# Optimization experiments

Measured on AMD Instinct MI355X. Metric: run time of the kernel, lower is better.

## Reference

```python
import jax, jax.numpy as jnp
import numpy as np

WH, WW = 16, 16          # window size
S = WH * WW              # tokens per window = 256
B = 128                  # batch of windows
E = 1024                 # embed_dim
H = 16                   # num_heads
D = E // H               # head_dim = 64


def _swin_rel_index():
    # Swin-style relative position index, identical to the torch buffer construction
    coords = np.stack(np.meshgrid(np.arange(WH), np.arange(WW), indexing='ij'))  # [2,WH,WW]
    cf = coords.reshape(2, -1)                         # [2, S]
    rel = cf[:, :, None] - cf[:, None, :]              # [2, S, S]
    rel = rel.transpose(1, 2, 0).copy()                # [S, S, 2]
    rel[..., 0] += WH - 1
    rel[..., 1] += WW - 1
    rel[..., 0] *= 2 * WW - 1
    return rel.sum(-1).astype(np.int32)                # [S, S] in [0, (2WH-1)(2WW-1))


def setup_inputs() -> dict:
    key = jax.random.key(0)
    ks = jax.random.split(key, 6)
    x = jax.random.normal(ks[0], (B, S, E), dtype=jnp.float32)
    qkv_w = jax.random.normal(ks[1], (3 * E, E), dtype=jnp.float32) * 0.02
    qkv_b = jax.random.normal(ks[2], (3 * E,), dtype=jnp.float32) * 0.02
    out_w = jax.random.normal(ks[3], (E, E), dtype=jnp.float32) * 0.02
    out_b = jax.random.normal(ks[4], (E,), dtype=jnp.float32) * 0.02
    bias_table = jax.random.normal(ks[5], ((2 * WH - 1) * (2 * WW - 1), H), dtype=jnp.float32) * 0.02
    rel_index = jnp.asarray(_swin_rel_index())
    return {"x": x, "qkv_w": qkv_w, "qkv_b": qkv_b, "out_w": out_w,
            "out_b": out_b, "bias_table": bias_table, "rel_index": rel_index,
            "x_ignored_": 0, "x_ignored_1_": 0}


def reference(x, qkv_w, qkv_b, out_w, out_b, bias_table, rel_index, x_ignored_, x_ignored_1_):
    b, s, e = x.shape
    h = bias_table.shape[-1]
    d = e // h
    # fused QKV projection
    qkv = x @ qkv_w.T + qkv_b                          # [b, s, 3e]
    qkv = qkv.reshape(b, s, 3, h, d)
    q, k, v = qkv[:, :, 0], qkv[:, :, 1], qkv[:, :, 2]  # [b, s, h, d]
    scale = d ** -0.5
    # learned relative position bias, [h, s, s]
    bias = bias_table[rel_index.reshape(-1)].reshape(s, s, h).transpose(2, 0, 1)
    scores = jnp.einsum('bqhd,bkhd->bhqk', q, k) * scale + bias[None]
    attn = jax.nn.softmax(scores, axis=-1)
    ctx = jnp.einsum('bhqk,bkhd->bqhd', attn, v).reshape(b, s, e)
    return ctx @ out_w.T + out_b
```

## Files before the change

### kernel.cpp

```cpp
#include <hip/hip_runtime.h>
#include <stdint.h>

#define BB 128
#define SS 256
#define EE 1024
#define HH 16
#define DD 64
#define MM (BB*SS)

#define LOG2E 1.44269504088896f

typedef __attribute__((ext_vector_type(8))) short bf16x8;
typedef __attribute__((ext_vector_type(4))) float f32x4;

__device__ __forceinline__ unsigned short f2bf(float f) {
  union { float f; unsigned int u; } c; c.f = f;
  unsigned int u = c.u;
  u += 0x7fffu + ((u >> 16) & 1u);
  return (unsigned short)(u >> 16);
}

__device__ __forceinline__ float fast_exp2(float x) {
#if __has_builtin(__builtin_amdgcn_exp2f)
  return __builtin_amdgcn_exp2f(x);
#else
  return exp2f(x);
#endif
}

__device__ __forceinline__ float fast_rcp(float x) {
#if __has_builtin(__builtin_amdgcn_rcpf)
  return __builtin_amdgcn_rcpf(x);
#else
  return 1.0f / x;
#endif
}

__device__ __forceinline__ void gld16(const unsigned short* g, unsigned short* l) {
  __builtin_amdgcn_global_load_lds((__attribute__((address_space(1))) void*)(g),
                                   (__attribute__((address_space(3))) void*)(l), 16, 0, 0);
}

__global__ __launch_bounds__(256) void prep_kernel(const float4* __restrict__ x4,
                                                   const float4* __restrict__ qw,
                                                   const float4* __restrict__ ow,
                                                   const float* __restrict__ btab,
                                                   const int* __restrict__ ridx,
                                                   ushort4* __restrict__ xb,
                                                   ushort4* __restrict__ qwb,
                                                   ushort4* __restrict__ owb,
                                                   float* __restrict__ biasC) {
  const int NX = (MM * EE) / 4;
  const int NQ = (3 * EE * EE) / 4;
  const int NO = (EE * EE) / 4;
  const int NBIAS = HH * SS * SS;
  const int total = NX + NQ + NO + NBIAS;
  int stride = gridDim.x * blockDim.x;
  for (int i = blockIdx.x * blockDim.x + threadIdx.x; i < total; i += stride) {
    if (i < NX) {
      float4 v = x4[i];
      ushort4 r; r.x = f2bf(v.x); r.y = f2bf(v.y); r.z = f2bf(v.z); r.w = f2bf(v.w);
      xb[i] = r;
    } else if (i < NX + NQ) {
      int t = i - NX;
      float4 v = qw[t];
      ushort4 r; r.x = f2bf(v.x); r.y = f2bf(v.y); r.z = f2bf(v.z); r.w = f2bf(v.w);
      qwb[t] = r;
    } else if (i < NX + NQ + NO) {
      int t = i - (NX + NQ);
      float4 v = ow[t];
      ushort4 r; r.x = f2bf(v.x); r.y = f2bf(v.y); r.z = f2bf(v.z); r.w = f2bf(v.w);
      owb[t] = r;
    } else {
      int t = i - (NX + NQ + NO);
      int h   = t >> 16;
      int row = (t >> 8) & 255;
      int lo  = (t >> 4) & 15;
      int hi  = t & 15;
      int col = hi * 16 + lo;
      biasC[t] = btab[ridx[row * SS + col] * HH + h] * LOG2E;
    }
  }
}

#define GEMM_NT 16

__device__ __forceinline__ void mfma16(f32x4& c, bf16x8 a, bf16x8 b) {
  c = __builtin_amdgcn_mfma_f32_16x16x32_bf16(a, b, c, 0, 0, 0);
}

#define STAGE_A(buf, kh, tt) do { \
    unsigned short* _d = S_A + ((buf)*2 + (kh))*8192; \
    gld16(srcA0 + (tt)*64 + (kh)*32, _d + ldso0); \
    gld16(srcA1 + (tt)*64 + (kh)*32, _d + ldso1); } while (0)
#define STAGE_B(buf, kh, tt) do { \
    unsigned short* _d = S_B + ((buf)*2 + (kh))*8192; \
    gld16(srcB0 + (tt)*64 + (kh)*32, _d + ldso0); \
    gld16(srcB1 + (tt)*64 + (kh)*32, _d + ldso1); } while (0)
#define LOAD_A8(buf, kh) do { \
    const unsigned short* _u = S_A + ((buf)*2 + (kh))*8192 + aoff; \
    _Pragma("unroll") for (int mi = 0; mi < 8; ++mi) \
      af[mi] = *(const bf16x8*)(_u + mi*512); } while (0)
#define LOAD_B2(buf, kh, nj0) do { \
    const unsigned short* _u = S_B + ((buf)*2 + (kh))*8192 + boff; \
    bfr[(nj0)]   = *(const bf16x8*)(_u + (nj0)*512); \
    bfr[(nj0)+1] = *(const bf16x8*)(_u + ((nj0)+1)*512); } while (0)
#define MFMA_Q(nj0) do { \
    _Pragma("unroll") for (int mi = 0; mi < 8; ++mi) { \
      mfma16(acc[mi][(nj0)],   af[mi], bfr[(nj0)]); \
      mfma16(acc[mi][(nj0)+1], af[mi], bfr[(nj0)+1]); } } while (0)
#define WAIT_LGKM0() do { asm volatile("s_waitcnt lgkmcnt(0)" ::: "memory"); \
                          __builtin_amdgcn_sched_barrier(0); } while (0)

__device__ __forceinline__ void gemm256_loop(const unsigned short* __restrict__ A,
                                             const unsigned short* __restrict__ Bw,
                                             unsigned short* S_A, unsigned short* S_B,
                                             int row0, int col0, f32x4 (&acc)[8][4]) {
  const int tid = threadIdx.x;
  const int wave = tid >> 6, lane = tid & 63;
  const int wm = wave >> 2, wn = wave & 3;
  const int l15 = lane & 15, quad = lane >> 4;
  const int cq = quad ^ ((l15 >> 1) & 3);
  const int aoff = (wm * 128 + l15) * 32 + cq * 8;
  const int boff = (wn * 64 + l15) * 32 + cq * 8;
  const int r0g = tid >> 2, c0g = tid & 3;
  const int gc = c0g ^ ((r0g >> 1) & 3);
  const unsigned short* srcA0 = A  + (size_t)(row0 + r0g) * EE + gc * 8;
  const unsigned short* srcA1 = A  + (size_t)(row0 + 128 + r0g) * EE + gc * 8;
  const unsigned short* srcB0 = Bw + (size_t)(col0 + r0g) * EE + gc * 8;
  const unsigned short* srcB1 = Bw + (size_t)(col0 + 128 + r0g) * EE + gc * 8;
  const int ldso0 = wave * 512;
  const int ldso1 = 4096 + wave * 512;

  STAGE_A(0, 0, 0); STAGE_B(0, 0, 0); STAGE_A(0, 1, 0); STAGE_B(0, 1, 0);
  STAGE_A(1, 0, 1); STAGE_B(1, 0, 1); STAGE_A(1, 1, 1);
  asm volatile("s_waitcnt vmcnt(6)" ::: "memory");
  __builtin_amdgcn_sched_barrier(0);
  __builtin_amdgcn_s_barrier();

  bf16x8 af[8], bfr[4];
  for (int t = 0; t < GEMM_NT; ++t) {
    const int d = t & 1;
    LOAD_A8(d, 0); LOAD_B2(d, 0, 0);
    if (t + 1 < GEMM_NT) STAGE_B(d ^ 1, 1, t + 1);
    __builtin_amdgcn_s_barrier();
    WAIT_LGKM0();
    __builtin_amdgcn_s_setprio(1);
    MFMA_Q(0);
    __builtin_amdgcn_s_setprio(0);
    __builtin_amdgcn_s_barrier();
    LOAD_B2(d, 0, 2);
    if (t + 2 < GEMM_NT) STAGE_A(d, 0, t + 2);
    __builtin_amdgcn_s_barrier();
    WAIT_LGKM0();
    __builtin_amdgcn_s_setprio(1);
    MFMA_Q(2);
    __builtin_amdgcn_s_setprio(0);
    __builtin_amdgcn_s_barrier();
    LOAD_A8(d, 1); LOAD_B2(d, 1, 0);
    if (t + 2 < GEMM_NT) STAGE_B(d, 0, t + 2);
    __builtin_amdgcn_s_barrier();
    WAIT_LGKM0();
    __builtin_amdgcn_s_setprio(1);
    MFMA_Q(0);
    __builtin_amdgcn_s_setprio(0);
    __builtin_amdgcn_s_barrier();
    LOAD_B2(d, 1, 2);
    if (t + 2 < GEMM_NT) STAGE_A(d, 1, t + 2);
    if (t < GEMM_NT - 2) { asm volatile("s_waitcnt vmcnt(6)" ::: "memory"); }
    else                 { asm volatile("s_waitcnt vmcnt(0)" ::: "memory"); }
    __builtin_amdgcn_sched_barrier(0);
    __builtin_amdgcn_s_barrier();
    WAIT_LGKM0();
    __builtin_amdgcn_s_setprio(1);
    MFMA_Q(2);
    __builtin_amdgcn_s_setprio(0);
    __builtin_amdgcn_s_barrier();
  }
}

__global__ __launch_bounds__(512, 2) void qkv_gemm(const unsigned short* __restrict__ A,
                                                   const unsigned short* __restrict__ Bw,
                                                   const float* __restrict__ bias,
                                                   unsigned short* __restrict__ q,
                                                   unsigned short* __restrict__ kx,
                                                   unsigned short* __restrict__ vt) {
  __shared__ unsigned short S_A[32768];
  __shared__ unsigned short S_B[32768];
  const int bid = blockIdx.x;
  const int swz = (bid & 7) * (gridDim.x >> 3) + (bid >> 3);
  const int row0 = (swz & 127) * 256;
  const int col0 = (swz >> 7) * 256;
  const int tid = threadIdx.x;
  const int wave = tid >> 6, lane = tid & 63;
  const int wm = wave >> 2, wn = wave & 3;
  const int l15 = lane & 15, quad = lane >> 4;
  f32x4 acc[8][4];
#pragma unroll
  for (int i = 0; i < 8; ++i)
#pragma unroll
    for (int j = 0; j < 4; ++j) acc[i][j] = (f32x4){0.f, 0.f, 0.f, 0.f};
  gemm256_loop(A, Bw, S_A, S_B, row0, col0, acc);
  const int which = col0 >> 10;
  const float QS = 0.125f * LOG2E;
#pragma unroll
  for (int mi = 0; mi < 8; ++mi) {
    const int m = row0 + wm * 128 + mi * 16 + quad * 4;
    const int bb = m >> 8;
    const int s0 = m & 255;
#pragma unroll
    for (int nj = 0; nj < 4; ++nj) {
      const int n = col0 + wn * 64 + nj * 16 + l15;
      const int hn = (n >> 6) & 15;
      const int dd2 = n & 63;
      const float bv = bias[n];
      if (which == 0) {
        size_t base = ((size_t)(bb * HH + hn) * SS + s0) * DD + dd2;
#pragma unroll
        for (int r = 0; r < 4; ++r)
          q[base + (size_t)r * DD] = f2bf((acc[mi][nj][r] + bv) * QS);
      } else if (which == 1) {
        size_t base = ((size_t)(bb * HH + hn) * SS + s0) * DD + dd2;
#pragma unroll
        for (int r = 0; r < 4; ++r)
          kx[base + (size_t)r * DD] = f2bf(acc[mi][nj][r] + bv);
      } else {
        size_t base = ((size_t)(bb * HH + hn) * DD + dd2) * SS + s0;
        ushort4 pk;
        pk.x = f2bf(acc[mi][nj][0] + bv);
        pk.y = f2bf(acc[mi][nj][1] + bv);
        pk.z = f2bf(acc[mi][nj][2] + bv);
        pk.w = f2bf(acc[mi][nj][3] + bv);
        *(ushort4*)(vt + base) = pk;
      }
    }
  }
}

__global__ __launch_bounds__(256) void attn_kernel(const unsigned short* __restrict__ q,
                                                   const unsigned short* __restrict__ kx,
                                                   const unsigned short* __restrict__ vt,
                                                   const float* __restrict__ biasC,
                                                   unsigned short* __restrict__ ctx) {
  __shared__ unsigned short Ks[256 * 64];
  __shared__ unsigned short P[4][16 * 256];
  const int tid = threadIdx.x;
  const int wave = tid >> 6, lane = tid & 63;
  const int l15 = lane & 15, quad = lane >> 4;
  const int swl = l15 & 7;
  const int bh = blockIdx.x;
  const int h = bh & 15;
  const int b_ = bh >> 4;
  const unsigned short* qp = q + (size_t)bh * SS * DD;
  const unsigned short* kp = kx + (size_t)bh * SS * DD;
  const unsigned short* vp = vt + (size_t)bh * SS * DD;

#pragma unroll
  for (int rr = 0; rr < 8; ++rr) {
    int gc = rr * 256 + tid;
    int row = gc >> 3, sc = gc & 7;
    int c = sc ^ (row & 7);
    gld16(kp + row * 64 + c * 8, Ks + (rr * 256 + wave * 64) * 8);
  }
  __syncthreads();

  unsigned short* Pw = &P[wave][0];
  for (int qblk = 0; qblk < 4; ++qblk) {
    const int qr0 = qblk * 64 + wave * 16;
    bf16x8 aq0 = *(const bf16x8*)(qp + (qr0 + l15) * DD + quad * 8);
    bf16x8 aq1 = *(const bf16x8*)(qp + (qr0 + l15) * DD + 32 + quad * 8);

    f32x4 sacc[16];
#pragma unroll
    for (int j = 0; j < 16; ++j) sacc[j] = (f32x4){0.f, 0.f, 0.f, 0.f};
#pragma unroll
    for (int j = 0; j < 16; ++j) {
      const unsigned short* krow = Ks + (j * 16 + l15) * 64;
      bf16x8 b0 = *(const bf16x8*)(krow + (quad ^ swl) * 8);
      bf16x8 b1 = *(const bf16x8*)(krow + ((4 + quad) ^ swl) * 8);
      sacc[j] = __builtin_amdgcn_mfma_f32_16x16x32_bf16(aq0, b0, sacc[j], 0, 0, 0);
      sacc[j] = __builtin_amdgcn_mfma_f32_16x16x32_bf16(aq1, b1, sacc[j], 0, 0, 0);
    }
#pragma unroll
    for (int r = 0; r < 4; ++r) {
      const int prow = quad * 4 + r;
      const float* bC = biasC + ((size_t)((h * 256 + qr0 + prow) * 16 + l15)) * 16;
      float4 bv0 = ((const float4*)bC)[0];
      float4 bv1 = ((const float4*)bC)[1];
      float4 bv2 = ((const float4*)bC)[2];
      float4 bv3 = ((const float4*)bC)[3];
      float bj[16] = {bv0.x, bv0.y, bv0.z, bv0.w, bv1.x, bv1.y, bv1.z, bv1.w,
                      bv2.x, bv2.y, bv2.z, bv2.w, bv3.x, bv3.y, bv3.z, bv3.w};
      float s = 0.f;
#pragma unroll
      for (int j = 0; j < 16; ++j) {
        float e = fast_exp2(sacc[j][r] + bj[j]);
        sacc[j][r] = e;
        s += e;
      }
#pragma unroll
      for (int m = 8; m >= 1; m >>= 1) s += __shfl_xor(s, m, 16);
      float rs = fast_rcp(s);
      const int psw = prow & 7;
#pragma unroll
      for (int j = 0; j < 16; ++j) {
        union { float f; unsigned int u; } cv; cv.f = sacc[j][r] * rs;
        unsigned short pb = (unsigned short)((cv.u + 0x8000u) >> 16);
        Pw[prow * 256 + (((2 * j + (l15 >> 3)) ^ psw) << 3) + swl] = pb;
      }
    }
    f32x4 cacc[4];
#pragma unroll
    for (int nt = 0; nt < 4; ++nt) cacc[nt] = (f32x4){0.f, 0.f, 0.f, 0.f};
#pragma unroll
    for (int kk = 0; kk < 8; ++kk) {
      bf16x8 a = *(const bf16x8*)(Pw + l15 * 256 + (((kk * 4 + quad) ^ swl) << 3));
#pragma unroll
      for (int nt = 0; nt < 4; ++nt) {
        bf16x8 b = *(const bf16x8*)(vp + (nt * 16 + l15) * SS + kk * 32 + quad * 8);
        cacc[nt] = __builtin_amdgcn_mfma_f32_16x16x32_bf16(a, b, cacc[nt], 0, 0, 0);
      }
    }
#pragma unroll
    for (int nt = 0; nt < 4; ++nt)
#pragma unroll
      for (int r = 0; r < 4; ++r)
        ctx[(size_t)(b_ * SS + qr0 + quad * 4 + r) * EE + h * DD + nt * 16 + l15] =
            f2bf(cacc[nt][r]);
  }
}

__global__ __launch_bounds__(512, 2) void out_gemm(const unsigned short* __restrict__ A,
                                                   const unsigned short* __restrict__ Bw,
                                                   const float* __restrict__ bias,
                                                   float* __restrict__ out) {
  __shared__ unsigned short S_A[32768];
  __shared__ unsigned short S_B[32768];
  const int bid = blockIdx.x;
  const int swz = (bid & 7) * (gridDim.x >> 3) + (bid >> 3);
  const int row0 = (swz & 127) * 256;
  const int col0 = (swz >> 7) * 256;
  const int tid = threadIdx.x;
  const int wave = tid >> 6, lane = tid & 63;
  const int wm = wave >> 2, wn = wave & 3;
  const int l15 = lane & 15, quad = lane >> 4;
  f32x4 acc[8][4];
#pragma unroll
  for (int i = 0; i < 8; ++i)
#pragma unroll
    for (int j = 0; j < 4; ++j) acc[i][j] = (f32x4){0.f, 0.f, 0.f, 0.f};
  gemm256_loop(A, Bw, S_A, S_B, row0, col0, acc);
#pragma unroll
  for (int mi = 0; mi < 8; ++mi) {
    const int m0 = row0 + wm * 128 + mi * 16 + quad * 4;
#pragma unroll
    for (int nj = 0; nj < 4; ++nj) {
      const int n = col0 + wn * 64 + nj * 16 + l15;
      const float bv = bias[n];
#pragma unroll
      for (int r = 0; r < 4; ++r)
        out[(size_t)(m0 + r) * EE + n] = acc[mi][nj][r] + bv;
    }
  }
}

#define WS_XCTX  ((size_t)0)
#define WS_QKVW  ((size_t)67108864)
#define WS_OUTW  ((size_t)73400320)
#define WS_BIAS  ((size_t)75497472)
#define WS_Q     ((size_t)79691776)
#define WS_K     ((size_t)146800640)
#define WS_VT    ((size_t)213909504)

extern "C" void kernel_launch(void* const* d_in, const int* in_sizes, int n_in,
                              void* d_out, int out_size, void* d_ws, size_t ws_size,
                              hipStream_t stream) {
  (void)in_sizes; (void)n_in; (void)out_size; (void)ws_size;
  const float* x      = (const float*)d_in[0];
  const float* qkv_w  = (const float*)d_in[1];
  const float* qkv_b  = (const float*)d_in[2];
  const float* out_w  = (const float*)d_in[3];
  const float* out_b  = (const float*)d_in[4];
  const float* btab   = (const float*)d_in[5];
  const int*   ridx   = (const int*)d_in[6];
  float* out = (float*)d_out;
  char* ws = (char*)d_ws;

  unsigned short* xctx  = (unsigned short*)(ws + WS_XCTX);
  unsigned short* qkvwb = (unsigned short*)(ws + WS_QKVW);
  unsigned short* outwb = (unsigned short*)(ws + WS_OUTW);
  float*          biasC = (float*)(ws + WS_BIAS);
  unsigned short* q     = (unsigned short*)(ws + WS_Q);
  unsigned short* k     = (unsigned short*)(ws + WS_K);
  unsigned short* vt    = (unsigned short*)(ws + WS_VT);

  prep_kernel<<<8192, 256, 0, stream>>>((const float4*)x, (const float4*)qkv_w,
                                        (const float4*)out_w, btab, ridx,
                                        (ushort4*)xctx, (ushort4*)qkvwb,
                                        (ushort4*)outwb, biasC);
  qkv_gemm<<<dim3((MM / 256) * ((3 * EE) / 256)), 512, 0, stream>>>(xctx, qkvwb, qkv_b,
                                                                    q, k, vt);
  attn_kernel<<<BB * HH, 256, 0, stream>>>(q, k, vt, biasC, xctx);
  out_gemm<<<dim3((MM / 256) * (EE / 256)), 512, 0, stream>>>(xctx, outwb, out_b, out);
}
```

Baseline: 777.1 us.

## Restructure GEMM main loop with inline-asm LDS reads and nontemporal epilogue stores

Reorganizes the shared 256x256 GEMM main loop so that each quarter-step loads A fragments for four rows across both k-halves, using inline-asm ds_read_b128 with immediate offsets. The global-to-LDS staging order is reshuffled, and both STAGE_A halves are now issued together after the third MFMA block. Epilogue stores for q, k, vt and out switch to nontemporal stores so the streaming outputs avoid polluting cache. The risk is that the hand-written LDS reads and reordered waitcnt/barrier placement could create hazards or stalls, and nontemporal stores may hurt reuse of q, k and v by the attention kernel.

```diff
diff --git a/kernel.cpp b/kernel.cpp
--- a/kernel.cpp
+++ b/kernel.cpp
@@ -12,6 +12,7 @@
 
 typedef __attribute__((ext_vector_type(8))) short bf16x8;
 typedef __attribute__((ext_vector_type(4))) float f32x4;
+typedef __attribute__((address_space(3))) unsigned short lds_us;
 
 __device__ __forceinline__ unsigned short f2bf(float f) {
   union { float f; unsigned int u; } c; c.f = f;
@@ -39,6 +40,13 @@
 __device__ __forceinline__ void gld16(const unsigned short* g, unsigned short* l) {
   __builtin_amdgcn_global_load_lds((__attribute__((address_space(1))) void*)(g),
                                    (__attribute__((address_space(3))) void*)(l), 16, 0, 0);
+}
+
+template <int OFF>
+__device__ __forceinline__ bf16x8 dsr128(const lds_us* p) {
+  bf16x8 r;
+  asm volatile("ds_read_b128 %0, %1 offset:%2" : "=&v"(r) : "v"(p), "i"(OFF));
+  return r;
 }
 
 __global__ __launch_bounds__(256) void prep_kernel(const float4* __restrict__ x4,
@@ -97,20 +105,19 @@
     unsigned short* _d = S_B + ((buf)*2 + (kh))*8192; \
     gld16(srcB0 + (tt)*64 + (kh)*32, _d + ldso0); \
     gld16(srcB1 + (tt)*64 + (kh)*32, _d + ldso1); } while (0)
-#define LOAD_A8(buf, kh) do { \
-    const unsigned short* _u = S_A + ((buf)*2 + (kh))*8192 + aoff; \
-    _Pragma("unroll") for (int mi = 0; mi < 8; ++mi) \
-      af[mi] = *(const bf16x8*)(_u + mi*512); } while (0)
-#define LOAD_B2(buf, kh, nj0) do { \
-    const unsigned short* _u = S_B + ((buf)*2 + (kh))*8192 + boff; \
-    bfr[(nj0)]   = *(const bf16x8*)(_u + (nj0)*512); \
-    bfr[(nj0)+1] = *(const bf16x8*)(_u + ((nj0)+1)*512); } while (0)
-#define MFMA_Q(nj0) do { \
-    _Pragma("unroll") for (int mi = 0; mi < 8; ++mi) { \
-      mfma16(acc[mi][(nj0)],   af[mi], bfr[(nj0)]); \
-      mfma16(acc[mi][(nj0)+1], af[mi], bfr[(nj0)+1]); } } while (0)
-#define WAIT_LGKM0() do { asm volatile("s_waitcnt lgkmcnt(0)" ::: "memory"); \
-                          __builtin_amdgcn_sched_barrier(0); } while (0)
+
+#define RAF(mi, kh, mbase) af[mi][kh] = dsr128<(kh)*16384 + ((mbase)+(mi))*1024>(aP)
+#define RBF(nj, kh)        bfr[nj][kh] = dsr128<(kh)*16384 + (nj)*1024>(bP)
+
+#define MF_Q(mi0, nj0) do { \
+    _Pragma("unroll") for (int kh = 0; kh < 2; ++kh) \
+    _Pragma("unroll") for (int mi = 0; mi < 4; ++mi) \
+    _Pragma("unroll") for (int nj = 0; nj < 2; ++nj) \
+      mfma16(acc[(mi0)+mi][(nj0)+nj], af[mi][kh], bfr[(nj0)+nj][kh]); } while (0)
+
+#define BAR() __builtin_amdgcn_s_barrier()
+#define WAITL0() do { asm volatile("s_waitcnt lgkmcnt(0)" ::: "memory"); \
+                      __builtin_amdgcn_sched_barrier(0); } while (0)
 
 __device__ __forceinline__ void gemm256_loop(const unsigned short* __restrict__ A,
                                              const unsigned short* __restrict__ Bw,
@@ -131,51 +138,56 @@
   const unsigned short* srcB1 = Bw + (size_t)(col0 + 128 + r0g) * EE + gc * 8;
   const int ldso0 = wave * 512;
   const int ldso1 = 4096 + wave * 512;
+  const lds_us* A3 = (const lds_us*)S_A;
+  const lds_us* B3 = (const lds_us*)S_B;
 
   STAGE_A(0, 0, 0); STAGE_B(0, 0, 0); STAGE_A(0, 1, 0); STAGE_B(0, 1, 0);
-  STAGE_A(1, 0, 1); STAGE_B(1, 0, 1); STAGE_A(1, 1, 1);
+  STAGE_A(1, 0, 1); STAGE_A(1, 1, 1); STAGE_B(1, 0, 1);
   asm volatile("s_waitcnt vmcnt(6)" ::: "memory");
   __builtin_amdgcn_sched_barrier(0);
-  __builtin_amdgcn_s_barrier();
-
-  bf16x8 af[8], bfr[4];
+  BAR();
+
+  bf16x8 af[4][2], bfr[4][2];
   for (int t = 0; t < GEMM_NT; ++t) {
     const int d = t & 1;
-    LOAD_A8(d, 0); LOAD_B2(d, 0, 0);
+    const lds_us* aP = A3 + (d << 14) + aoff;
+    const lds_us* bP = B3 + (d << 14) + boff;
+    RAF(0, 0, 0); RAF(1, 0, 0); RAF(2, 0, 0); RAF(3, 0, 0);
+    RAF(0, 1, 0); RAF(1, 1, 0); RAF(2, 1, 0); RAF(3, 1, 0);
+    RBF(0, 0); RBF(1, 0); RBF(0, 1); RBF(1, 1);
     if (t + 1 < GEMM_NT) STAGE_B(d ^ 1, 1, t + 1);
-    __builtin_amdgcn_s_barrier();
-    WAIT_LGKM0();
+    asm volatile("s_waitcnt lgkmcnt(8)" ::: "memory");
+    BAR();
+    WAITL0();
     __builtin_amdgcn_s_setprio(1);
-    MFMA_Q(0);
+    MF_Q(0, 0);
     __builtin_amdgcn_s_setprio(0);
-    __builtin_amdgcn_s_barrier();
-    LOAD_B2(d, 0, 2);
-    if (t + 2 < GEMM_NT) STAGE_A(d, 0, t + 2);
-    __builtin_amdgcn_s_barrier();
-    WAIT_LGKM0();
+    BAR();
+    RBF(2, 0); RBF(3, 0); RBF(2, 1); RBF(3, 1);
+    BAR();
+    WAITL0();
     __builtin_amdgcn_s_setprio(1);
-    MFMA_Q(2);
+    MF_Q(0, 2);
     __builtin_amdgcn_s_setprio(0);
-    __builtin_amdgcn_s_barrier();
-    LOAD_A8(d, 1); LOAD_B2(d, 1, 0);
+    BAR();
+    RAF(0, 0, 4); RAF(1, 0, 4); RAF(2, 0, 4); RAF(3, 0, 4);
+    RAF(0, 1, 4); RAF(1, 1, 4); RAF(2, 1, 4); RAF(3, 1, 4);
     if (t + 2 < GEMM_NT) STAGE_B(d, 0, t + 2);
-    __builtin_amdgcn_s_barrier();
-    WAIT_LGKM0();
+    BAR();
+    WAITL0();
     __builtin_amdgcn_s_setprio(1);
-    MFMA_Q(0);
+    MF_Q(4, 0);
     __builtin_amdgcn_s_setprio(0);
-    __builtin_amdgcn_s_barrier();
-    LOAD_B2(d, 1, 2);
-    if (t + 2 < GEMM_NT) STAGE_A(d, 1, t + 2);
+    BAR();
+    if (t + 2 < GEMM_NT) { STAGE_A(d, 0, t + 2); STAGE_A(d, 1, t + 2); }
     if (t < GEMM_NT - 2) { asm volatile("s_waitcnt vmcnt(6)" ::: "memory"); }
     else                 { asm volatile("s_waitcnt vmcnt(0)" ::: "memory"); }
     __builtin_amdgcn_sched_barrier(0);
-    __builtin_amdgcn_s_barrier();
-    WAIT_LGKM0();
+    BAR();
     __builtin_amdgcn_s_setprio(1);
-    MFMA_Q(2);
+    MF_Q(4, 2);
     __builtin_amdgcn_s_setprio(0);
-    __builtin_amdgcn_s_barrier();
+    BAR();
   }
 }
 
@@ -218,20 +230,20 @@
         size_t base = ((size_t)(bb * HH + hn) * SS + s0) * DD + dd2;
 #pragma unroll
         for (int r = 0; r < 4; ++r)
-          q[base + (size_t)r * DD] = f2bf((acc[mi][nj][r] + bv) * QS);
+          __builtin_nontemporal_store(f2bf((acc[mi][nj][r] + bv) * QS), &q[base + (size_t)r * DD]);
       } else if (which == 1) {
         size_t base = ((size_t)(bb * HH + hn) * SS + s0) * DD + dd2;
 #pragma unroll
         for (int r = 0; r < 4; ++r)
-          kx[base + (size_t)r * DD] = f2bf(acc[mi][nj][r] + bv);
+          __builtin_nontemporal_store(f2bf(acc[mi][nj][r] + bv), &kx[base + (size_t)r * DD]);
       } else {
         size_t base = ((size_t)(bb * HH + hn) * DD + dd2) * SS + s0;
-        ushort4 pk;
-        pk.x = f2bf(acc[mi][nj][0] + bv);
-        pk.y = f2bf(acc[mi][nj][1] + bv);
-        pk.z = f2bf(acc[mi][nj][2] + bv);
-        pk.w = f2bf(acc[mi][nj][3] + bv);
-        *(ushort4*)(vt + base) = pk;
+        unsigned long long pv =
+            (unsigned long long)f2bf(acc[mi][nj][0] + bv) |
+            ((unsigned long long)f2bf(acc[mi][nj][1] + bv) << 16) |
+            ((unsigned long long)f2bf(acc[mi][nj][2] + bv) << 32) |
+            ((unsigned long long)f2bf(acc[mi][nj][3] + bv) << 48);
+        __builtin_nontemporal_store(pv, (unsigned long long*)(vt + base));
       }
     }
   }
@@ -359,7 +371,7 @@
       const float bv = bias[n];
 #pragma unroll
       for (int r = 0; r < 4; ++r)
-        out[(size_t)(m0 + r) * EE + n] = acc[mi][nj][r] + bv;
+        __builtin_nontemporal_store(acc[mi][nj][r] + bv, &out[(size_t)(m0 + r) * EE + n]);
     }
   }
 }
```

Result: slower. 822.6 us (+5.9%).
